# Kernel optimization log

Measured on AMD Instinct MI355X. Metric: run time of the kernel, lower is better.

Reference implementation:

```python
import jax, jax.numpy as jnp
import numpy as np

N_GROUP = 64
GROUP_SIZE = 64
INPUT_DIM = 2048
BATCH = 8192
N_MONTN = 512


def setup_inputs() -> dict:
    key = jax.random.key(0)
    k1, k2, k3, k4, k5 = jax.random.split(key, 5)
    x = jax.random.normal(k1, (BATCH, INPUT_DIM), dtype=jnp.float32)
    weight = jax.random.normal(k2, (N_GROUP * GROUP_SIZE, INPUT_DIM), dtype=jnp.float32) * 0.02
    bias = jax.random.normal(k3, (N_GROUP * GROUP_SIZE,), dtype=jnp.float32) * 0.02
    rand_u = jax.random.uniform(k4, (BATCH,), dtype=jnp.float32)
    montn_index = jax.random.randint(k5, (N_MONTN,), 0, INPUT_DIM, dtype=jnp.int32)
    return {"x": x, "weight": weight, "bias": bias, "rand_u": rand_u,
            "montn_index": montn_index}


def reference(x, weight, bias, rand_u, montn_index):
    # Square the weights on monotone input columns (in-place in torch).
    w = weight.at[:, montn_index].set(weight[:, montn_index] ** 2)
    # y = x @ w^T + b  -> [B, n_group * n_group_size]
    y = jnp.einsum('bi,oi->bo', x, w) + bias
    B = y.shape[0]
    # per-group min over contiguous slices, then max over groups
    group_mins = y.reshape(B, N_GROUP, GROUP_SIZE).min(axis=2)  # [B, n_group]
    out = group_mins.max(axis=1)                                 # [B]
    # vectorized Bernoulli: 1.0 if u < sigmoid(out) else 0.0
    sample = (rand_u < jax.nn.sigmoid(out)).astype(jnp.float32)
    return sample.reshape(-1, 1)
```

## Files before the change

### kernel.cpp

```cpp
#include <hip/hip_runtime.h>
#include <cmath>


typedef _Float16 f16x8 __attribute__((ext_vector_type(8)));
typedef float f32x4 __attribute__((ext_vector_type(4)));

#define MARGIN_EPS 4e-3f
#define MAX_UNDEC 96

__device__ __forceinline__ void async_load16(const void* gptr, void* lptr) {
  __builtin_amdgcn_global_load_lds(
      (const __attribute__((address_space(1))) void*)gptr,
      (__attribute__((address_space(3))) void*)lptr, 16, 0, 0);
}

__device__ __forceinline__ float us2f(unsigned short u) {
  return (float)__builtin_bit_cast(_Float16, u);
}

__global__ void convert_split(float* __restrict__ x, float* __restrict__ wgt,
                              const int* __restrict__ montn,
                              int* __restrict__ count) {
  __shared__ unsigned msk[64];
  const int t = threadIdx.x, l = t & 63, w = t >> 6;
  const int r = blockIdx.x * 4 + w;
  const int use_mask = (r >= 8192) ? 1 : 0;
  if (blockIdx.x == 0 && t == 0) *count = 0;
  if (use_mask) {
    if (t < 64) msk[t] = 0u;
    __syncthreads();
    for (int j = t; j < 512; j += 256) {
      const int c = montn[j];
      atomicOr(&msk[c >> 5], 1u << (c & 31));
    }
    __syncthreads();
  }
  float* rowp = use_mask ? (wgt + (size_t)(r - 8192) * 2048)
                         : (x + (size_t)r * 2048);
  float4 v[8];
#pragma unroll
  for (int j = 0; j < 8; ++j) v[j] = ((const float4*)rowp)[l + 64 * j];
  unsigned mw[8];
#pragma unroll
  for (int j = 0; j < 8; ++j)
    mw[j] = use_mask ? msk[(l >> 3) + 8 * j] : 0u;

  unsigned short* up = (unsigned short*)rowp;
#pragma unroll
  for (int j = 0; j < 8; ++j) {
    unsigned short hs[4], ls[4];
    const float* fv = (const float*)&v[j];
#pragma unroll
    for (int c = 0; c < 4; ++c) {
      float f = fv[c];
      if ((mw[j] >> (4 * (l & 7) + c)) & 1u) f = f * f;
      _Float16 h = (_Float16)f;
      float res = f - (float)h;
      _Float16 lo = (_Float16)res;
      hs[c] = __builtin_bit_cast(unsigned short, h);
      ls[c] = __builtin_bit_cast(unsigned short, lo);
    }
    uint2 H, L;
    H.x = (unsigned)hs[0] | ((unsigned)hs[1] << 16);
    H.y = (unsigned)hs[2] | ((unsigned)hs[3] << 16);
    L.x = (unsigned)ls[0] | ((unsigned)ls[1] << 16);
    L.y = (unsigned)ls[2] | ((unsigned)ls[3] << 16);
    *((uint2*)(up + 4 * l + 256 * j)) = H;
    *((uint2*)(up + 2048 + 4 * l + 256 * j)) = L;
  }
}

__global__ __launch_bounds__(256, 4) void gemm_minmax(
    const unsigned short* __restrict__ X, const unsigned short* __restrict__ W,
    const float* __restrict__ bias, float* __restrict__ gmins) {
  __shared__ unsigned short As[128 * 64];
  __shared__ unsigned short Bs[128 * 64];
  const int t = threadIdx.x;
  const int lane = t & 63;
  const int w = t >> 6;
  const int wm = w >> 1, wn = w & 1;
  const int lin = blockIdx.x;
  const int sid = lin >> 3;
  const int m0 = (sid >> 2) * 128;
  const int n0 = ((lin & 7) * 4 + (sid & 3)) * 128;

  const int rowBase = w * 8 + (lane >> 3);
  const int gchunk = ((lane & 7) ^ ((lane >> 3) & 7)) * 8;
  size_t sA[4], sB[4];
#pragma unroll
  for (int c = 0; c < 4; ++c) {
    sA[c] = (size_t)(m0 + c * 32 + rowBase) * 4096 + gchunk;
    sB[c] = (size_t)(n0 + c * 32 + rowBase) * 4096 + gchunk;
  }
  unsigned short* ldsA[4];
  unsigned short* ldsB[4];
#pragma unroll
  for (int c = 0; c < 4; ++c) {
    ldsA[c] = As + c * 2048 + w * 512;
    ldsB[c] = Bs + c * 2048 + w * 512;
  }

  const int am = lane & 15, quad = lane >> 4;
  int arow[4], brow[4];
#pragma unroll
  for (int i = 0; i < 4; ++i) {
    arow[i] = (wm * 64 + i * 16 + am) * 64;
    brow[i] = (wn * 64 + i * 16 + am) * 64;
  }
  int swz[2];
#pragma unroll
  for (int h = 0; h < 2; ++h) swz[h] = (((h << 2) + quad) ^ (am & 7)) * 8;

  f32x4 acc[4][4];
#pragma unroll
  for (int i = 0; i < 4; ++i)
#pragma unroll
    for (int j = 0; j < 4; ++j) acc[i][j] = (f32x4){0.f, 0.f, 0.f, 0.f};

#pragma unroll 1
  for (int it = 0; it < 32; ++it) {
    const int kin = it * 64;
    __syncthreads();
#pragma unroll
    for (int c = 0; c < 4; ++c) {
      async_load16(X + sA[c] + kin, ldsA[c]);
      async_load16(W + sB[c] + kin, ldsB[c]);
    }
    __syncthreads();

#pragma unroll
    for (int h = 0; h < 2; ++h) {
      f16x8 av[4], bv[4];
#pragma unroll
      for (int i = 0; i < 4; ++i) av[i] = *(const f16x8*)(As + arow[i] + swz[h]);
#pragma unroll
      for (int i = 0; i < 4; ++i) bv[i] = *(const f16x8*)(Bs + brow[i] + swz[h]);
#pragma unroll
      for (int mb = 0; mb < 4; ++mb)
#pragma unroll
        for (int nb = 0; nb < 4; ++nb)
          acc[mb][nb] = __builtin_amdgcn_mfma_f32_16x16x32_f16(
              av[mb], bv[nb], acc[mb][nb], 0, 0, 0);
    }
  }

  float bv4[4];
#pragma unroll
  for (int nb = 0; nb < 4; ++nb) bv4[nb] = bias[n0 + wn * 64 + nb * 16 + am];
  const int grp = (n0 >> 6) + wn;
#pragma unroll
  for (int mb = 0; mb < 4; ++mb) {
#pragma unroll
    for (int reg = 0; reg < 4; ++reg) {
      float v = fminf(fminf(acc[mb][0][reg] + bv4[0], acc[mb][1][reg] + bv4[1]),
                      fminf(acc[mb][2][reg] + bv4[2], acc[mb][3][reg] + bv4[3]));
      v = fminf(v, __shfl_xor(v, 1, 64));
      v = fminf(v, __shfl_xor(v, 2, 64));
      v = fminf(v, __shfl_xor(v, 4, 64));
      v = fminf(v, __shfl_xor(v, 8, 64));
      if (am == 0) {
        const int row = m0 + wm * 64 + mb * 16 + quad * 4 + reg;
        gmins[(size_t)row * 64 + grp] = v;
      }
    }
  }
}

__global__ void finalize_margin(const float* __restrict__ gmins,
                                const float* __restrict__ rand_u,
                                float* __restrict__ out,
                                int* __restrict__ count, int* __restrict__ undec,
                                float4* __restrict__ ybuf4) {
  if (blockIdx.x < 384)
    ybuf4[(size_t)blockIdx.x * 256 + threadIdx.x] = (float4){0.f, 0.f, 0.f, 0.f};
  const int wv = threadIdx.x >> 6, lane = threadIdx.x & 63;
  const int row = blockIdx.x * 4 + wv;
  float v = gmins[(size_t)row * 64 + lane];
  v = fmaxf(v, __shfl_xor(v, 1, 64));
  v = fmaxf(v, __shfl_xor(v, 2, 64));
  v = fmaxf(v, __shfl_xor(v, 4, 64));
  v = fmaxf(v, __shfl_xor(v, 8, 64));
  v = fmaxf(v, __shfl_xor(v, 16, 64));
  v = fmaxf(v, __shfl_xor(v, 32, 64));
  if (lane == 0) {
    const float u = rand_u[row];
    const float slo = 1.0f / (1.0f + expf(-(v - MARGIN_EPS)));
    const float shi = 1.0f / (1.0f + expf(-(v + MARGIN_EPS)));
    if (u < slo) {
      out[row] = 1.0f;
    } else if (u >= shi) {
      out[row] = 0.0f;
    } else {
      const int i = atomicAdd(count, 1);
      if (i < 8192) undec[i] = row;
    }
  }
}

__global__ __launch_bounds__(256) void recompute_rows(
    const unsigned short* __restrict__ X, const unsigned short* __restrict__ W,
    const int* __restrict__ count, const int* __restrict__ undec,
    float* __restrict__ ybuf) {
  __shared__ float wf[64 * 129];
  __shared__ float part[256];
  const int g = blockIdx.x, kc = blockIdx.y;
  const int t = threadIdx.x;
  int n = *count;
  if (n > MAX_UNDEC) n = MAX_UNDEC;
  if (n == 0) return;

  {
    const int cl = t >> 2, ks = t & 3;
    const unsigned short* wp =
        W + (size_t)(g * 64 + cl) * 4096 + kc * 128 + ks * 32;
    float* dst = wf + cl * 129 + ks * 32;
#pragma unroll
    for (int i = 0; i < 32; i += 8) {
      uint4 hv = *(const uint4*)(wp + i);
      uint4 lv = *(const uint4*)(wp + 2048 + i);
      const unsigned* hw = (const unsigned*)&hv;
      const unsigned* lw = (const unsigned*)&lv;
#pragma unroll
      for (int m = 0; m < 4; ++m) {
        dst[i + 2 * m] = us2f((unsigned short)(hw[m] & 0xFFFF)) +
                         us2f((unsigned short)(lw[m] & 0xFFFF));
        dst[i + 2 * m + 1] = us2f((unsigned short)(hw[m] >> 16)) +
                             us2f((unsigned short)(lw[m] >> 16));
      }
    }
  }
  __syncthreads();

  const int col = t & 63, kq = t >> 6;
  const float* wcol = wf + col * 129 + kq * 32;
  for (int s = 0; s < n; ++s) {
    const int row = undec[s];
    const unsigned short* xp = X + (size_t)row * 4096 + kc * 128 + kq * 32;
    float acc = 0.f;
#pragma unroll
    for (int i = 0; i < 32; i += 8) {
      uint4 hv = *(const uint4*)(xp + i);
      uint4 lv = *(const uint4*)(xp + 2048 + i);
      const unsigned* hw = (const unsigned*)&hv;
      const unsigned* lw = (const unsigned*)&lv;
#pragma unroll
      for (int m = 0; m < 4; ++m) {
        const float x0 = us2f((unsigned short)(hw[m] & 0xFFFF)) +
                         us2f((unsigned short)(lw[m] & 0xFFFF));
        const float x1 = us2f((unsigned short)(hw[m] >> 16)) +
                         us2f((unsigned short)(lw[m] >> 16));
        acc = fmaf(x0, wcol[i + 2 * m], acc);
        acc = fmaf(x1, wcol[i + 2 * m + 1], acc);
      }
    }
    part[t] = acc;
    __syncthreads();
    if (t < 64) {
      const float y = part[t] + part[t + 64] + part[t + 128] + part[t + 192];
      atomicAdd(ybuf + (size_t)s * 4096 + g * 64 + t, y);
    }
    __syncthreads();
  }
}

__global__ void decide(const float* __restrict__ ybuf,
                       const int* __restrict__ undec, const int* __restrict__ count,
                       const float* __restrict__ bias,
                       const float* __restrict__ rand_u, float* __restrict__ out) {
  __shared__ float gm[64];
  int n = *count;
  if (n > MAX_UNDEC) n = MAX_UNDEC;
  const int s = blockIdx.x;
  if (s >= n) return;
  const int t = threadIdx.x;
  const int g = t >> 2, p4 = t & 3;
  const float* yb = ybuf + (size_t)s * 4096;
  const int c0 = g * 64 + p4 * 16;
  float m = 3.4e38f;
#pragma unroll
  for (int e = 0; e < 16; ++e) m = fminf(m, yb[c0 + e] + bias[c0 + e]);
  m = fminf(m, __shfl_xor(m, 1, 64));
  m = fminf(m, __shfl_xor(m, 2, 64));
  if (p4 == 0) gm[g] = m;
  __syncthreads();
  if (t < 64) {
    float v = gm[t];
    v = fmaxf(v, __shfl_xor(v, 1, 64));
    v = fmaxf(v, __shfl_xor(v, 2, 64));
    v = fmaxf(v, __shfl_xor(v, 4, 64));
    v = fmaxf(v, __shfl_xor(v, 8, 64));
    v = fmaxf(v, __shfl_xor(v, 16, 64));
    v = fmaxf(v, __shfl_xor(v, 32, 64));
    if (t == 0) {
      const int row = undec[s];
      const float sg = 1.0f / (1.0f + expf(-v));
      out[row] = (rand_u[row] < sg) ? 1.0f : 0.0f;
    }
  }
}

extern "C" void kernel_launch(void* const* d_in, const int* in_sizes, int n_in,
                              void* d_out, int out_size, void* d_ws, size_t ws_size,
                              hipStream_t stream) {
  float* x = (float*)d_in[0];
  float* weight = (float*)d_in[1];
  const float* bias = (const float*)d_in[2];
  const float* rand_u = (const float*)d_in[3];
  const int* montn = (const int*)d_in[4];
  float* out = (float*)d_out;

  char* ws = (char*)d_ws;
  int* count = (int*)ws;
  int* undec = (int*)(ws + 256);
  float* ybuf = (float*)(ws + 65536);
  float* gmins = (float*)(ws + 65536 + 1572864);

  convert_split<<<3072, 256, 0, stream>>>(x, weight, montn, count);
  gemm_minmax<<<2048, 256, 0, stream>>>(
      (const unsigned short*)x, (const unsigned short*)weight, bias, gmins);
  finalize_margin<<<2048, 256, 0, stream>>>(gmins, rand_u, out, count, undec,
                                            (float4*)ybuf);
  recompute_rows<<<dim3(64, 16), 256, 0, stream>>>(
      (const unsigned short*)x, (const unsigned short*)weight, count, undec, ybuf);
  decide<<<MAX_UNDEC, 256, 0, stream>>>(ybuf, undec, count, bias, rand_u, out);
}
```

Baseline: 291.0 us.

## Load W fragments directly into registers with double buffering, keep only X in LDS

```diff
diff --git a/kernel.cpp b/kernel.cpp
--- a/kernel.cpp
+++ b/kernel.cpp
@@ -70,11 +70,10 @@
   }
 }
 
-__global__ __launch_bounds__(256, 4) void gemm_minmax(
+__global__ __launch_bounds__(256, 3) void gemm_minmax(
     const unsigned short* __restrict__ X, const unsigned short* __restrict__ W,
     const float* __restrict__ bias, float* __restrict__ gmins) {
   __shared__ unsigned short As[128 * 64];
-  __shared__ unsigned short Bs[128 * 64];
   const int t = threadIdx.x;
   const int lane = t & 63;
   const int w = t >> 6;
@@ -86,63 +85,78 @@
 
   const int rowBase = w * 8 + (lane >> 3);
   const int gchunk = ((lane & 7) ^ ((lane >> 3) & 7)) * 8;
-  size_t sA[4], sB[4];
+  size_t sA[4];
+  unsigned short* ldsA[4];
 #pragma unroll
   for (int c = 0; c < 4; ++c) {
     sA[c] = (size_t)(m0 + c * 32 + rowBase) * 4096 + gchunk;
-    sB[c] = (size_t)(n0 + c * 32 + rowBase) * 4096 + gchunk;
-  }
-  unsigned short* ldsA[4];
-  unsigned short* ldsB[4];
-#pragma unroll
-  for (int c = 0; c < 4; ++c) {
     ldsA[c] = As + c * 2048 + w * 512;
-    ldsB[c] = Bs + c * 2048 + w * 512;
   }
 
   const int am = lane & 15, quad = lane >> 4;
-  int arow[4], brow[4];
-#pragma unroll
-  for (int i = 0; i < 4; ++i) {
-    arow[i] = (wm * 64 + i * 16 + am) * 64;
-    brow[i] = (wn * 64 + i * 16 + am) * 64;
-  }
+  int arow[4];
+#pragma unroll
+  for (int i = 0; i < 4; ++i) arow[i] = (wm * 64 + i * 16 + am) * 64;
   int swz[2];
 #pragma unroll
   for (int h = 0; h < 2; ++h) swz[h] = (((h << 2) + quad) ^ (am & 7)) * 8;
 
+  const unsigned short* bp[4];
+#pragma unroll
+  for (int i = 0; i < 4; ++i)
+    bp[i] = W + (size_t)(n0 + wn * 64 + i * 16 + am) * 4096 + quad * 8;
+
   f32x4 acc[4][4];
 #pragma unroll
   for (int i = 0; i < 4; ++i)
 #pragma unroll
     for (int j = 0; j < 4; ++j) acc[i][j] = (f32x4){0.f, 0.f, 0.f, 0.f};
 
+#define STAGE_A(IT)                                                    \
+  {                                                                    \
+    _Pragma("unroll") for (int c = 0; c < 4; ++c)                      \
+        async_load16(X + sA[c] + (IT) * 64, ldsA[c]);                  \
+  }
+#define LOAD_B(BREG, IT)                                               \
+  {                                                                    \
+    _Pragma("unroll") for (int i = 0; i < 4; ++i) {                    \
+      BREG[i][0] = *(const f16x8*)(bp[i] + (IT) * 64);                 \
+      BREG[i][1] = *(const f16x8*)(bp[i] + (IT) * 64 + 32);            \
+    }                                                                  \
+  }
+#define COMPUTE_STEP(BREG)                                             \
+  {                                                                    \
+    _Pragma("unroll") for (int h = 0; h < 2; ++h) {                    \
+      f16x8 av[4];                                                     \
+      _Pragma("unroll") for (int i = 0; i < 4; ++i)                    \
+          av[i] = *(const f16x8*)(As + arow[i] + swz[h]);              \
+      _Pragma("unroll") for (int mb = 0; mb < 4; ++mb)                 \
+          _Pragma("unroll") for (int nb = 0; nb < 4; ++nb)             \
+              acc[mb][nb] = __builtin_amdgcn_mfma_f32_16x16x32_f16(    \
+                  av[mb], BREG[nb][h], acc[mb][nb], 0, 0, 0);          \
+    }                                                                  \
+  }
+
+  f16x8 b0[4][2], b1[4][2];
+  LOAD_B(b0, 0);
+
 #pragma unroll 1
-  for (int it = 0; it < 32; ++it) {
-    const int kin = it * 64;
-    __syncthreads();
-#pragma unroll
-    for (int c = 0; c < 4; ++c) {
-      async_load16(X + sA[c] + kin, ldsA[c]);
-      async_load16(W + sB[c] + kin, ldsB[c]);
-    }
-    __syncthreads();
-
-#pragma unroll
-    for (int h = 0; h < 2; ++h) {
-      f16x8 av[4], bv[4];
-#pragma unroll
-      for (int i = 0; i < 4; ++i) av[i] = *(const f16x8*)(As + arow[i] + swz[h]);
-#pragma unroll
-      for (int i = 0; i < 4; ++i) bv[i] = *(const f16x8*)(Bs + brow[i] + swz[h]);
-#pragma unroll
-      for (int mb = 0; mb < 4; ++mb)
-#pragma unroll
-        for (int nb = 0; nb < 4; ++nb)
-          acc[mb][nb] = __builtin_amdgcn_mfma_f32_16x16x32_f16(
-              av[mb], bv[nb], acc[mb][nb], 0, 0, 0);
-    }
-  }
+  for (int p = 0; p < 16; ++p) {
+    const int it0 = 2 * p, it1 = 2 * p + 1;
+    __syncthreads();
+    STAGE_A(it0);
+    LOAD_B(b1, it1);
+    __syncthreads();
+    COMPUTE_STEP(b0);
+    __syncthreads();
+    STAGE_A(it1);
+    if (p < 15) LOAD_B(b0, it1 + 1);
+    __syncthreads();
+    COMPUTE_STEP(b1);
+  }
+#undef STAGE_A
+#undef LOAD_B
+#undef COMPUTE_STEP
 
   float bv4[4];
 #pragma unroll
```

After: 432.5 us. 48.7% more time.
